# Kernel tuning notes

Measured on AMD Instinct MI355X. Metric: run time of the kernel, lower is better.

Reference implementation:

```python
import jax, jax.numpy as jnp
import numpy as np

NUM_HEADS = 16
HEAD_DIM = 64
EPS = 1e-6


def rms_norm(x, w):
    # normalize in float32, cast back (matches torch RMSNorm.forward)
    xf = x.astype(jnp.float32)
    y = xf * jax.lax.rsqrt(jnp.mean(xf * xf, axis=-1, keepdims=True) + EPS)
    return y.astype(x.dtype) * w


def setup_inputs() -> dict:
    key = jax.random.key(0)
    ks = jax.random.split(key, 5)
    B, N, C = 2, 2048, 1024
    x = jax.random.normal(ks[0], (B, N, C), dtype=jnp.float32)
    w_qkv = jax.random.normal(ks[1], (3 * C, C), dtype=jnp.float32) * (1.0 / np.sqrt(C))
    b_qkv = jax.random.normal(ks[2], (3 * C,), dtype=jnp.float32) * 0.02
    q_norm_w = jnp.ones((HEAD_DIM,), dtype=jnp.float32)
    k_norm_w = jnp.ones((HEAD_DIM,), dtype=jnp.float32)
    w_proj = jax.random.normal(ks[3], (C, C), dtype=jnp.float32) * (1.0 / np.sqrt(C))
    b_proj = jax.random.normal(ks[4], (C,), dtype=jnp.float32) * 0.02
    return {"x": x, "w_qkv": w_qkv, "b_qkv": b_qkv, "q_norm_w": q_norm_w,
            "k_norm_w": k_norm_w, "w_proj": w_proj, "b_proj": b_proj}


def reference(x, w_qkv, b_qkv, q_norm_w, k_norm_w, w_proj, b_proj):
    B, N, C = x.shape
    H, D = NUM_HEADS, HEAD_DIM
    scale = D ** -0.5
    # fused QKV projection: [B,N,3C]
    qkv = jnp.einsum('bnc,oc->bno', x, w_qkv) + b_qkv
    qkv = qkv.reshape(B, N, 3, H, D)
    q = qkv[:, :, 0].transpose(0, 2, 1, 3)  # [B,H,N,D]
    k = qkv[:, :, 1].transpose(0, 2, 1, 3)
    v = qkv[:, :, 2].transpose(0, 2, 1, 3)
    q = rms_norm(q, q_norm_w)
    k = rms_norm(k, k_norm_w)
    # SDPA (no causal mask, no dropout)
    scores = jnp.einsum('bhqd,bhkd->bhqk', q, k) * scale
    attn = jax.nn.softmax(scores, axis=-1)
    out = jnp.einsum('bhqk,bhkd->bhqd', attn, v)  # [B,H,N,D]
    out = out.transpose(0, 2, 1, 3).reshape(B, N, C)
    return jnp.einsum('bnc,oc->bno', out, w_proj) + b_proj
```

## Files before the change

### kernel.cpp

```cpp
#include <hip/hip_runtime.h>
#include <hip/hip_bf16.h>

typedef __attribute__((ext_vector_type(8))) short short8;
typedef __attribute__((ext_vector_type(8))) unsigned short ushort8;
typedef __attribute__((ext_vector_type(4))) float f32x4;
typedef __attribute__((ext_vector_type(4))) unsigned short u16x4;

#define MFMA16(a, b, c) __builtin_amdgcn_mfma_f32_16x16x32_bf16(a, b, c, 0, 0, 0)

__device__ __forceinline__ unsigned short f2bf(float f) {
  union { float f; unsigned u; } x; x.f = f;
  unsigned r = x.u + 0x7FFFu + ((x.u >> 16) & 1u);
  return (unsigned short)(r >> 16);
}
__device__ __forceinline__ float bf2f(unsigned short h) {
  union { unsigned u; float f; } x; x.u = ((unsigned)h) << 16;
  return x.f;
}
__device__ __forceinline__ void load_lds16(const void* g, void* l) {
  __builtin_amdgcn_global_load_lds((const __attribute__((address_space(1))) void*)g,
                                   (__attribute__((address_space(3))) void*)l, 16, 0, 0);
}

__global__ __launch_bounds__(256) void convert_all(
    const float* __restrict__ x, const float* __restrict__ wqkv, const float* __restrict__ wproj,
    unsigned short* __restrict__ xb, unsigned short* __restrict__ wqkvb,
    unsigned short* __restrict__ wprojb) {
  int i = blockIdx.x * 256 + threadIdx.x;
  const float4* src; unsigned short* dst; int o;
  if (i < 1048576) { src = (const float4*)x; dst = xb; o = i; }
  else if (i < 1048576 + 786432) { src = (const float4*)wqkv; dst = wqkvb; o = i - 1048576; }
  else { src = (const float4*)wproj; dst = wprojb; o = i - (1048576 + 786432); }
  float4 v = src[o];
  u16x4 r; r.x = f2bf(v.x); r.y = f2bf(v.y); r.z = f2bf(v.z); r.w = f2bf(v.w);
  *(u16x4*)(dst + (size_t)o * 4) = r;
}

template <int MODE>
__global__ __launch_bounds__(256) void gemm_nt(
    const unsigned short* __restrict__ A, const unsigned short* __restrict__ Bm,
    const float* __restrict__ bias, void* __restrict__ Cout, int M, int N, int K,
    const float* __restrict__ qnw, const float* __restrict__ knw,
    unsigned short* __restrict__ vT) {
  __shared__ unsigned short As[128 * 32];
  __shared__ unsigned short Bs[128 * 32];
  const int t = threadIdx.x, w = t >> 6, l = t & 63;
  const int la = l & 15, lg = l >> 4;
  const int wm = w >> 1, wn = w & 1;
  const int m0 = blockIdx.y * 128, n0 = blockIdx.x * 128;

  const int r0 = t >> 2, c0 = (t & 3) ^ ((r0 >> 1) & 3);
  const int r1 = r0 + 64, c1 = (t & 3) ^ ((r1 >> 1) & 3);
  const unsigned short* a0 = A + (size_t)(m0 + r0) * K + c0 * 8;
  const unsigned short* a1 = A + (size_t)(m0 + r1) * K + c1 * 8;
  const unsigned short* b0 = Bm + (size_t)(n0 + r0) * K + c0 * 8;
  const unsigned short* b1 = Bm + (size_t)(n0 + r1) * K + c1 * 8;
  char* ldsA0 = (char*)As + w * 1024;
  char* ldsA1 = (char*)As + w * 1024 + 4096;
  char* ldsB0 = (char*)Bs + w * 1024;
  char* ldsB1 = (char*)Bs + w * 1024 + 4096;

  f32x4 acc[4][4] = {};
  int offA[4], offB[4];
#pragma unroll
  for (int f = 0; f < 4; ++f) {
    int ra = wm * 64 + f * 16 + la;
    offA[f] = ra * 64 + ((lg ^ ((ra >> 1) & 3)) * 16);
    int rb = wn * 64 + f * 16 + la;
    offB[f] = rb * 64 + ((lg ^ ((rb >> 1) & 3)) * 16);
  }

  for (int kt = 0; kt < K; kt += 32) {
    __syncthreads();
    load_lds16(a0 + kt, ldsA0);
    load_lds16(a1 + kt, ldsA1);
    load_lds16(b0 + kt, ldsB0);
    load_lds16(b1 + kt, ldsB1);
    __syncthreads();
    short8 af[4], bf[4];
#pragma unroll
    for (int f = 0; f < 4; ++f) af[f] = *(const short8*)((const char*)As + offA[f]);
#pragma unroll
    for (int f = 0; f < 4; ++f) bf[f] = *(const short8*)((const char*)Bs + offB[f]);
#pragma unroll
    for (int mf = 0; mf < 4; ++mf)
#pragma unroll
      for (int nf = 0; nf < 4; ++nf)
        acc[mf][nf] = MFMA16(af[mf], bf[nf], acc[mf][nf]);
  }

  const int colb = n0 + wn * 64 + la;
  const int rowb = m0 + wm * 64 + lg * 4;

#pragma unroll
  for (int nf = 0; nf < 4; ++nf) {
    const float bv = bias[colb + nf * 16];
#pragma unroll
    for (int mf = 0; mf < 4; ++mf)
#pragma unroll
      for (int r = 0; r < 4; ++r) acc[mf][nf][r] += bv;
  }

  if (MODE == 0) {
#pragma unroll
    for (int nf = 0; nf < 4; ++nf) {
      const int col = colb + nf * 16;
#pragma unroll
      for (int mf = 0; mf < 4; ++mf)
#pragma unroll
        for (int r = 0; r < 4; ++r)
          ((float*)Cout)[(size_t)(rowb + mf * 16 + r) * N + col] = acc[mf][nf][r];
    }
  } else {
    const int part = n0 >> 10;
    if (part < 2) {
      const float* nw = part ? knw : qnw;
      float nwv[4];
#pragma unroll
      for (int nf = 0; nf < 4; ++nf) nwv[nf] = nw[la + nf * 16];
#pragma unroll
      for (int mf = 0; mf < 4; ++mf)
#pragma unroll
        for (int r = 0; r < 4; ++r) {
          float ss = acc[mf][0][r] * acc[mf][0][r];
#pragma unroll
          for (int nf = 1; nf < 4; ++nf) ss = __builtin_fmaf(acc[mf][nf][r], acc[mf][nf][r], ss);
          ss += __shfl_xor(ss, 1); ss += __shfl_xor(ss, 2);
          ss += __shfl_xor(ss, 4); ss += __shfl_xor(ss, 8);
          const float rs = rsqrtf(ss * (1.f / 64.f) + 1e-6f);
#pragma unroll
          for (int nf = 0; nf < 4; ++nf) acc[mf][nf][r] *= rs * nwv[nf];
        }
    }
    if (part < 2) {
#pragma unroll
      for (int nf = 0; nf < 4; ++nf) {
        const int col = colb + nf * 16;
#pragma unroll
        for (int mf = 0; mf < 4; ++mf)
#pragma unroll
          for (int r = 0; r < 4; ++r)
            ((unsigned short*)Cout)[(size_t)(rowb + mf * 16 + r) * N + col] = f2bf(acc[mf][nf][r]);
      }
    } else {
#pragma unroll
      for (int nf = 0; nf < 4; ++nf) {
        const int col = colb + nf * 16;
        const int h = (col >> 6) & 15;
        const int d = la + nf * 16;
#pragma unroll
        for (int mf = 0; mf < 4; ++mf) {
          const int row = rowb + mf * 16;
          const int b = row >> 11, n = row & 2047;
          u16x4 o;
#pragma unroll
          for (int r = 0; r < 4; ++r) o[r] = f2bf(acc[mf][nf][r]);
          *(u16x4*)(vT + ((size_t)(b * 16 + h) * 64 + d) * 2048 + n) = o;
        }
      }
    }
  }
}

__global__ __launch_bounds__(256) void attn_fwd(
    const unsigned short* __restrict__ qkv, const unsigned short* __restrict__ vT,
    unsigned short* __restrict__ outb) {
  __shared__ unsigned short Ks[64 * 64];
  __shared__ unsigned short Vs[64 * 64];
  __shared__ unsigned short Ps[4][16][76];
  const int t = threadIdx.x, w = t >> 6, l = t & 63;
  const int la = l & 15, lg = l >> 4;
  const int q0 = blockIdx.x * 64, bh = blockIdx.y;
  const int b = bh >> 4, h = bh & 15;

  const int qrow = q0 + w * 16 + la;
  const unsigned short* qp = qkv + (size_t)(b * 2048 + qrow) * 3072 + h * 64;
  const short8 qa0 = *(const short8*)(qp + lg * 8);
  const short8 qa1 = *(const short8*)(qp + 32 + lg * 8);

  const int r0 = t >> 3, c0 = (t & 7) ^ (r0 & 7);
  const int r1 = r0 + 32, c1 = (t & 7) ^ (r1 & 7);
  const unsigned short* k0p = qkv + (size_t)(b * 2048 + r0) * 3072 + 1024 + h * 64 + c0 * 8;
  const unsigned short* k1p = qkv + (size_t)(b * 2048 + r1) * 3072 + 1024 + h * 64 + c1 * 8;
  const unsigned short* v0p = vT + (size_t)(bh * 64 + r0) * 2048 + c0 * 8;
  const unsigned short* v1p = vT + (size_t)(bh * 64 + r1) * 2048 + c1 * 8;

  f32x4 accO[4] = {};
  float lsum = 0.f;
  const float SC = 0.125f * 1.44269504f;
  const float M = 12.0f;

  for (int kb = 0; kb < 2048; kb += 64) {
    __syncthreads();
    load_lds16(k0p + (size_t)kb * 3072, (char*)Ks + w * 1024);
    load_lds16(k1p + (size_t)kb * 3072, (char*)Ks + w * 1024 + 4096);
    load_lds16(v0p + kb, (char*)Vs + w * 1024);
    load_lds16(v1p + kb, (char*)Vs + w * 1024 + 4096);
    __syncthreads();

    f32x4 s[4] = {};
#pragma unroll
    for (int nf = 0; nf < 4; ++nf) {
      const int kr = nf * 16 + la;
      const short8 kf0 = *(const short8*)((const char*)Ks + kr * 128 + ((lg ^ (kr & 7)) * 16));
      const short8 kf1 = *(const short8*)((const char*)Ks + kr * 128 + (((4 + lg) ^ (kr & 7)) * 16));
      s[nf] = MFMA16(kf0, qa0, s[nf]);
      s[nf] = MFMA16(kf1, qa1, s[nf]);
    }
#pragma unroll
    for (int nf = 0; nf < 4; ++nf) {
      float e[4];
#pragma unroll
      for (int r = 0; r < 4; ++r)
        e[r] = __builtin_amdgcn_exp2f(__builtin_fmaf(s[nf][r], SC, -M));
      lsum += (e[0] + e[1]) + (e[2] + e[3]);
      union { __hip_bfloat162 hh[2]; u16x4 v; } pk;
      pk.hh[0] = __float22bfloat162_rn(float2{e[0], e[1]});
      pk.hh[1] = __float22bfloat162_rn(float2{e[2], e[3]});
      *(u16x4*)&Ps[w][la][nf * 16 + lg * 4] = pk.v;
    }
    asm volatile("" ::: "memory");
    const short8 pa0 = *(const short8*)&Ps[w][la][lg * 8];
    const short8 pa1 = *(const short8*)&Ps[w][la][32 + lg * 8];

#pragma unroll
    for (int df = 0; df < 4; ++df) {
      const int vr = df * 16 + la;
      const short8 vf0 = *(const short8*)((const char*)Vs + vr * 128 + ((lg ^ (vr & 7)) * 16));
      const short8 vf1 = *(const short8*)((const char*)Vs + vr * 128 + (((4 + lg) ^ (vr & 7)) * 16));
      accO[df] = MFMA16(pa0, vf0, accO[df]);
      accO[df] = MFMA16(pa1, vf1, accO[df]);
    }
  }
  lsum += __shfl_xor(lsum, 16);
  lsum += __shfl_xor(lsum, 32);
#pragma unroll
  for (int r = 0; r < 4; ++r) {
    const float inv = 1.f / __shfl(lsum, lg * 4 + r);
    const int orow = q0 + w * 16 + lg * 4 + r;
    unsigned short* op = outb + (size_t)(b * 2048 + orow) * 1024 + h * 64 + la;
#pragma unroll
    for (int df = 0; df < 4; ++df) op[df * 16] = f2bf(accO[df][r] * inv);
  }
}

extern "C" void kernel_launch(void* const* d_in, const int* in_sizes, int n_in,
                              void* d_out, int out_size, void* d_ws, size_t ws_size,
                              hipStream_t stream) {
  const float* x     = (const float*)d_in[0];
  const float* wqkv  = (const float*)d_in[1];
  const float* bqkv  = (const float*)d_in[2];
  const float* qnw   = (const float*)d_in[3];
  const float* knw   = (const float*)d_in[4];
  const float* wproj = (const float*)d_in[5];
  const float* bproj = (const float*)d_in[6];

  char* p = (char*)d_ws;
  unsigned short* xb     = (unsigned short*)p; p += (size_t)4096 * 1024 * 2;
  unsigned short* wqkvb  = (unsigned short*)p; p += (size_t)3072 * 1024 * 2;
  unsigned short* wprojb = (unsigned short*)p; p += (size_t)1024 * 1024 * 2;
  unsigned short* qkvb   = (unsigned short*)p; p += (size_t)4096 * 3072 * 2;
  unsigned short* vT     = (unsigned short*)p; p += (size_t)32 * 64 * 2048 * 2;
  unsigned short* aout   = (unsigned short*)p; p += (size_t)4096 * 1024 * 2;

  convert_all<<<8192, 256, 0, stream>>>(x, wqkv, wproj, xb, wqkvb, wprojb);
  gemm_nt<1><<<dim3(24, 32), 256, 0, stream>>>(xb, wqkvb, bqkv, qkvb, 4096, 3072, 1024,
                                               qnw, knw, vT);
  attn_fwd<<<dim3(32, 32), 256, 0, stream>>>(qkvb, vT, aout);
  gemm_nt<0><<<dim3(8, 32), 256, 0, stream>>>(aout, wprojb, bproj, d_out, 4096, 1024, 1024,
                                              nullptr, nullptr, nullptr);
}
```

Baseline: 131.6 us.

## Split attention over two key halves and add a combine kernel

```diff
diff --git a/kernel.cpp b/kernel.cpp
--- a/kernel.cpp
+++ b/kernel.cpp
@@ -131,8 +131,6 @@
 #pragma unroll
           for (int nf = 0; nf < 4; ++nf) acc[mf][nf][r] *= rs * nwv[nf];
         }
-    }
-    if (part < 2) {
 #pragma unroll
       for (int nf = 0; nf < 4; ++nf) {
         const int col = colb + nf * 16;
@@ -164,13 +162,13 @@
 
 __global__ __launch_bounds__(256) void attn_fwd(
     const unsigned short* __restrict__ qkv, const unsigned short* __restrict__ vT,
-    unsigned short* __restrict__ outb) {
+    float* __restrict__ pO, float* __restrict__ pL) {
   __shared__ unsigned short Ks[64 * 64];
   __shared__ unsigned short Vs[64 * 64];
   __shared__ unsigned short Ps[4][16][76];
   const int t = threadIdx.x, w = t >> 6, l = t & 63;
   const int la = l & 15, lg = l >> 4;
-  const int q0 = blockIdx.x * 64, bh = blockIdx.y;
+  const int q0 = blockIdx.x * 64, bh = blockIdx.y, kh = blockIdx.z;
   const int b = bh >> 4, h = bh & 15;
 
   const int qrow = q0 + w * 16 + la;
@@ -190,7 +188,8 @@
   const float SC = 0.125f * 1.44269504f;
   const float M = 12.0f;
 
-  for (int kb = 0; kb < 2048; kb += 64) {
+  const int kbBeg = kh << 10, kbEnd = kbBeg + 1024;
+  for (int kb = kbBeg; kb < kbEnd; kb += 64) {
     __syncthreads();
     load_lds16(k0p + (size_t)kb * 3072, (char*)Ks + w * 1024);
     load_lds16(k1p + (size_t)kb * 3072, (char*)Ks + w * 1024 + 4096);
@@ -234,14 +233,35 @@
   }
   lsum += __shfl_xor(lsum, 16);
   lsum += __shfl_xor(lsum, 32);
+  const size_t base = ((size_t)(kh * 32 + bh) * 2048);
+  if (lg == 0) pL[base + q0 + w * 16 + la] = lsum;
 #pragma unroll
   for (int r = 0; r < 4; ++r) {
-    const float inv = 1.f / __shfl(lsum, lg * 4 + r);
     const int orow = q0 + w * 16 + lg * 4 + r;
-    unsigned short* op = outb + (size_t)(b * 2048 + orow) * 1024 + h * 64 + la;
-#pragma unroll
-    for (int df = 0; df < 4; ++df) op[df * 16] = f2bf(accO[df][r] * inv);
-  }
+    float* op = pO + (base + orow) * 64 + la;
+#pragma unroll
+    for (int df = 0; df < 4; ++df) op[df * 16] = accO[df][r];
+  }
+}
+
+__global__ __launch_bounds__(256) void attn_combine(
+    const float* __restrict__ pO, const float* __restrict__ pL,
+    unsigned short* __restrict__ outb) {
+  const int u = blockIdx.x * 256 + threadIdx.x;
+  const int bhn = u >> 3, d8 = u & 7;
+  const int bh = bhn >> 11, n = bhn & 2047;
+  const int b = bh >> 4, h = bh & 15;
+  const float* a0 = pO + (size_t)bhn * 64 + d8 * 8;
+  const float* a1 = a0 + (size_t)32 * 2048 * 64;
+  const float inv = 1.f / (pL[bhn] + pL[bhn + 32 * 2048]);
+  float4 x0 = *(const float4*)a0, x1 = *(const float4*)(a0 + 4);
+  float4 y0 = *(const float4*)a1, y1 = *(const float4*)(a1 + 4);
+  ushort8 o;
+  o[0] = f2bf((x0.x + y0.x) * inv); o[1] = f2bf((x0.y + y0.y) * inv);
+  o[2] = f2bf((x0.z + y0.z) * inv); o[3] = f2bf((x0.w + y0.w) * inv);
+  o[4] = f2bf((x1.x + y1.x) * inv); o[5] = f2bf((x1.y + y1.y) * inv);
+  o[6] = f2bf((x1.z + y1.z) * inv); o[7] = f2bf((x1.w + y1.w) * inv);
+  *(ushort8*)(outb + (size_t)(b * 2048 + n) * 1024 + h * 64 + d8 * 8) = o;
 }
 
 extern "C" void kernel_launch(void* const* d_in, const int* in_sizes, int n_in,
@@ -262,11 +282,14 @@
   unsigned short* qkvb   = (unsigned short*)p; p += (size_t)4096 * 3072 * 2;
   unsigned short* vT     = (unsigned short*)p; p += (size_t)32 * 64 * 2048 * 2;
   unsigned short* aout   = (unsigned short*)p; p += (size_t)4096 * 1024 * 2;
+  float*          pO     = (float*)p;          p += (size_t)2 * 32 * 2048 * 64 * 4;
+  float*          pL     = (float*)p;          p += (size_t)2 * 32 * 2048 * 4;
 
   convert_all<<<8192, 256, 0, stream>>>(x, wqkv, wproj, xb, wqkvb, wprojb);
   gemm_nt<1><<<dim3(24, 32), 256, 0, stream>>>(xb, wqkvb, bqkv, qkvb, 4096, 3072, 1024,
                                                qnw, knw, vT);
-  attn_fwd<<<dim3(32, 32), 256, 0, stream>>>(qkvb, vT, aout);
+  attn_fwd<<<dim3(32, 32, 2), 256, 0, stream>>>(qkvb, vT, pO, pL);
+  attn_combine<<<2048, 256, 0, stream>>>(pO, pL, aout);
   gemm_nt<0><<<dim3(8, 32), 256, 0, stream>>>(aout, wprojb, bproj, d_out, 4096, 1024, 1024,
                                               nullptr, nullptr, nullptr);
 }
```

Result: slower. 139.0 us (+5.6%).
